# Performance work log

Measured on AMD Instinct MI355X. Metric: run time of the kernel, lower is better.

## Reference

```python
import jax, jax.numpy as jnp
import numpy as np

N, E, D = 50000, 800000, 128
H, C = 8, 16  # heads, hidden_per_head; H*C == D
NEG_SLOPE = 0.15


def setup_inputs() -> dict:
    key = jax.random.key(0)
    ks = jax.random.split(key, 8)
    x = jax.random.normal(ks[0], (N, D), dtype=jnp.float32)
    edge_index = jax.random.randint(ks[1], (2, E), 0, N, dtype=jnp.int32)
    s = 1.0 / np.sqrt(D)
    return {
        "x": x,
        "edge_index": edge_index,
        "ln_g": jnp.ones((D,), jnp.float32),
        "ln_b": jnp.zeros((D,), jnp.float32),
        "W_l": jax.random.normal(ks[2], (D, H * C), jnp.float32) * s,
        "b_l": jnp.zeros((H * C,), jnp.float32),
        "W_r": jax.random.normal(ks[3], (D, H * C), jnp.float32) * s,
        "b_r": jnp.zeros((H * C,), jnp.float32),
        "att": jax.random.normal(ks[4], (H, C), jnp.float32) * (1.0 / np.sqrt(C)),
        "bias": jnp.zeros((H * C,), jnp.float32),
    }


def _layernorm(x, g, b, eps=1e-5):
    mu = jnp.mean(x, axis=-1, keepdims=True)
    var = jnp.mean(jnp.square(x - mu), axis=-1, keepdims=True)
    return (x - mu) * jax.lax.rsqrt(var + eps) * g + b


def reference(x, edge_index, ln_g, ln_b, W_l, b_l, W_r, b_r, att, bias):
    src, dst = edge_index[0], edge_index[1]
    h = _layernorm(x, ln_g, ln_b)                      # [N, D]
    xl = (h @ W_l + b_l).reshape(N, H, C)              # source-side transform
    xr = (h @ W_r + b_r).reshape(N, H, C)              # target-side transform
    # GATv2 edge attention: leaky_relu(x_j + x_i) . att
    e = xl[src] + xr[dst]                              # [E, H, C]
    e_act = jnp.where(e > 0, e, NEG_SLOPE * e)
    alpha = jnp.einsum('ehc,hc->eh', e_act, att)       # [E, H]
    # segment softmax over edges grouped by destination node
    m = jax.ops.segment_max(alpha, dst, num_segments=N)   # [N, H]
    ex = jnp.exp(alpha - m[dst])                           # [E, H]
    denom = jax.ops.segment_sum(ex, dst, num_segments=N)  # [N, H]
    a = ex / (denom[dst] + 1e-16)                          # [E, H]
    # weighted message aggregation (scatter-add)
    msg = xl[src] * a[:, :, None]                          # [E, H, C]
    out = jax.ops.segment_sum(msg, dst, num_segments=N)   # [N, H, C]
    out = out.reshape(N, H * C) + bias
    h2 = jax.nn.relu(out)                                  # act='relu', dropout off (eval)
    return x + h2                                          # proj is Identity (in_dim == out_dim)
```

## Files before the change

### kernel.cpp

```cpp
#include <hip/hip_runtime.h>

typedef unsigned int uint32;
typedef __attribute__((ext_vector_type(4))) float f32x4;
typedef __attribute__((ext_vector_type(2))) float f32x2;
typedef __attribute__((ext_vector_type(8))) short bf16x8;

#define NEG_SLOPE 0.15f
#define GPB 2

__device__ __forceinline__ float2 bf2_to_f2(uint32 u) {
  union { uint32 i; float f; } a, b;
  a.i = u << 16;
  b.i = u & 0xffff0000u;
  return make_float2(a.f, b.f);
}

__device__ __forceinline__ f32x2 unpk(uint32 u) {
  union { uint32 i; float f; } lo, hi;
  lo.i = u << 16; hi.i = u & 0xffff0000u;
  f32x2 r; r.x = lo.f; r.y = hi.f; return r;
}

__device__ __forceinline__ float bf_to_f(unsigned short s) {
  union { uint32 i; float f; } u;
  u.i = ((uint32)s) << 16;
  return u.f;
}

__device__ __forceinline__ unsigned short f32_to_bf16(float f) {
  union { float f; uint32 i; } u; u.f = f;
  uint32 r = u.i + 0x7fffu + ((u.i >> 16) & 1u);
  return (unsigned short)(r >> 16);
}

__device__ __forceinline__ uint32 pack_bf2(float x, float y) {
  return (uint32)f32_to_bf16(x) | ((uint32)f32_to_bf16(y) << 16);
}

__device__ __forceinline__ float2 loadpair(const void* p, size_t i, int isbf) {
  if (isbf) return bf2_to_f2(((const uint32*)p)[i]);
  return ((const float2*)p)[i];
}

__device__ __forceinline__ float loadelem(const void* p, size_t i, int isbf) {
  if (isbf) return bf_to_f(((const unsigned short*)p)[i]);
  return ((const float*)p)[i];
}

__device__ __forceinline__ int get_isbf(const void* ln_g) {
  return ((const uint32*)ln_g)[0] != 0x3F800000u ? 1 : 0;
}

__device__ __forceinline__ float dpp_swap1(float x) {
  union { float f; int i; } u, r;
  u.f = x;
  r.i = __builtin_amdgcn_mov_dpp(u.i, 0xB1, 0xF, 0xF, false);
  return r.f;
}

__device__ __forceinline__ f32x2 pk_add(f32x2 a, f32x2 b) {
  f32x2 d;
  asm("v_pk_add_f32 %0, %1, %2" : "=v"(d) : "v"(a), "v"(b));
  return d;
}
__device__ __forceinline__ f32x2 pk_mul(f32x2 a, f32x2 b) {
  f32x2 d;
  asm("v_pk_mul_f32 %0, %1, %2" : "=v"(d) : "v"(a), "v"(b));
  return d;
}
__device__ __forceinline__ f32x2 pk_fma(f32x2 a, f32x2 b, f32x2 c) {
  f32x2 d;
  asm("v_pk_fma_f32 %0, %1, %2, %3" : "=v"(d) : "v"(a), "v"(b), "v"(c));
  return d;
}
__device__ __forceinline__ float exp2_raw(float x) {
  float r;
  asm("v_exp_f32 %0, %1" : "=v"(r) : "v"(x));
  return r;
}

__global__ __launch_bounds__(256) void prep_hist_k(
    const void* __restrict__ Wl, const void* __restrict__ Wr,
    const void* __restrict__ bl, const void* __restrict__ br,
    const void* __restrict__ att, const void* __restrict__ obias,
    const void* __restrict__ ln_g, const void* __restrict__ ln_b,
    unsigned short* __restrict__ Wt, float* __restrict__ c1,
    float* __restrict__ c2b, float* __restrict__ att_c,
    float* __restrict__ obias_c,
    const int* __restrict__ ei, int* __restrict__ cntg,
    int E, int Eb, int R)
{
  int b = blockIdx.x;
  if (b < 128) {
    int isbf = get_isbf(ln_g);
    int id = b * 256 + threadIdx.x;
    int n = id >> 7, k = id & 127;
    float g = loadelem(ln_g, k, isbf);
    float v = (n < 128) ? loadelem(Wl, (size_t)k * 128 + n, isbf)
                        : loadelem(Wr, (size_t)k * 128 + (n - 128), isbf);
    Wt[(size_t)n * 128 + k] = f32_to_bf16(g * v);
    if (id < 128) {
      att_c[id]   = loadelem(att, id, isbf) * 1.44269504088896f;
      obias_c[id] = loadelem(obias, id, isbf);
    }
  } else if (b < 192) {
    int isbf = get_isbf(ln_g);
    int w = threadIdx.x >> 6, lane = threadIdx.x & 63;
    int n = (b - 128) * 4 + w;
    const void* W = (n < 128) ? Wl : Wr;
    int nn = n & 127;
    float s1 = 0.f, s2 = 0.f;
    #pragma unroll
    for (int t = 0; t < 2; ++t) {
      int kk = t * 64 + lane;
      float wv = loadelem(W, (size_t)kk * 128 + nn, isbf);
      s1 += loadelem(ln_g, kk, isbf) * wv;
      s2 += loadelem(ln_b, kk, isbf) * wv;
    }
    #pragma unroll
    for (int off = 1; off < 64; off <<= 1) {
      s1 += __shfl_xor(s1, off, 64);
      s2 += __shfl_xor(s2, off, 64);
    }
    if (lane == 0) {
      c1[n] = s1;
      c2b[n] = s2 + ((n < 128) ? loadelem(bl, nn, isbf) : loadelem(br, nn, isbf));
    }
  } else {
    __shared__ int hist[256];
    int hb = b - 192, tid = threadIdx.x;
    hist[tid] = 0;
    __syncthreads();
    int startE = hb * Eb, endE = min(E, startE + Eb);
    const int* dp = ei + E;
    int nfull = (endE > startE) ? ((endE - startE) >> 2) : 0;
    for (int g = tid; g < nfull; g += 256) {
      int4 d = *(const int4*)(dp + startE + g * 4);
      atomicAdd(&hist[((uint32)d.x) >> 8], 1);
      atomicAdd(&hist[((uint32)d.y) >> 8], 1);
      atomicAdd(&hist[((uint32)d.z) >> 8], 1);
      atomicAdd(&hist[((uint32)d.w) >> 8], 1);
    }
    int rem0 = startE + nfull * 4;
    if (rem0 + tid < endE) atomicAdd(&hist[((uint32)dp[rem0 + tid]) >> 8], 1);
    __syncthreads();
    if (tid < R) cntg[tid * 256 + hb] = hist[tid];
  }
}

__global__ __launch_bounds__(1024) void scanA_k(const int* __restrict__ in,
    int* __restrict__ outl, int* __restrict__ psum, int n)
{
  __shared__ int wsum[16];
  int tid = threadIdx.x, lane = tid & 63, w = tid >> 6;
  int i = blockIdx.x * 1024 + tid;
  int v = (i < n) ? in[i] : 0;
  int xs = v;
  #pragma unroll
  for (int off = 1; off < 64; off <<= 1) {
    int y = __shfl_up(xs, off, 64);
    if (lane >= off) xs += y;
  }
  if (lane == 63) wsum[w] = xs;
  __syncthreads();
  if (w == 0) {
    int sv = (lane < 16) ? wsum[lane] : 0;
    int ss = sv;
    #pragma unroll
    for (int off = 1; off < 16; off <<= 1) {
      int y = __shfl_up(ss, off, 64);
      if (lane >= off) ss += y;
    }
    if (lane < 16) wsum[lane] = ss - sv;
    if (lane == 15) psum[blockIdx.x] = ss;
  }
  __syncthreads();
  if (i < n) outl[i] = wsum[w] + xs - v;
}

__device__ __forceinline__ void load_group(bf16x8* slot, const void* x,
                                           int isbf, int rl, int quad) {
  if (isbf) {
    const unsigned short* xp = (const unsigned short*)x + (size_t)rl * 128 + quad * 8;
    #pragma unroll
    for (int kc = 0; kc < 4; ++kc) slot[kc] = *(const bf16x8*)(xp + kc * 32);
  } else {
    const float* xp = (const float*)x + (size_t)rl * 128 + quad * 8;
    #pragma unroll
    for (int kc = 0; kc < 4; ++kc) {
      float4 a0 = *(const float4*)(xp + kc * 32);
      float4 a1 = *(const float4*)(xp + kc * 32 + 4);
      union { bf16x8 v; uint32 u[4]; } av;
      av.u[0] = pack_bf2(a0.x, a0.y);
      av.u[1] = pack_bf2(a0.z, a0.w);
      av.u[2] = pack_bf2(a1.x, a1.y);
      av.u[3] = pack_bf2(a1.z, a1.w);
      slot[kc] = av.v;
    }
  }
}

__global__ __launch_bounds__(256) void bin_gemm_k(
    const int* __restrict__ ei, const int* __restrict__ cbase,
    const int* __restrict__ psum, uint32* __restrict__ binned,
    int E, int Eb, int R, int nbScan,
    const void* __restrict__ x, const void* __restrict__ ln_g,
    const unsigned short* __restrict__ Wt,
    const float* __restrict__ c1, const float* __restrict__ c2b,
    unsigned short* __restrict__ xl, unsigned short* __restrict__ xr,
    int nrows)
{
  if (blockIdx.x < 256) {
    __shared__ int cur[256];
    __shared__ int spsum[64];
    int b = blockIdx.x, tid = threadIdx.x;
    if (tid < 64) {
      int v = (tid < nbScan) ? psum[tid] : 0;
      int xs = v;
      #pragma unroll
      for (int off = 1; off < 64; off <<= 1) {
        int y = __shfl_up(xs, off, 64);
        if (tid >= off) xs += y;
      }
      spsum[tid] = xs - v;
    }
    __syncthreads();
    if (tid < R) {
      int idx = tid * 256 + b;
      cur[tid] = cbase[idx] + spsum[idx >> 10];
    }
    __syncthreads();
    int startE = b * Eb, endE = min(E, startE + Eb);
    int nfull = (endE > startE) ? ((endE - startE) >> 2) : 0;
    for (int g = tid; g < nfull; g += 256) {
      int e = startE + g * 4;
      int4 s = *(const int4*)(ei + e);
      int4 d = *(const int4*)(ei + E + e);
      int p0 = atomicAdd(&cur[((uint32)d.x) >> 8], 1);
      binned[p0] = (uint32)s.x | (((uint32)d.x & 255u) << 16);
      int p1 = atomicAdd(&cur[((uint32)d.y) >> 8], 1);
      binned[p1] = (uint32)s.y | (((uint32)d.y & 255u) << 16);
      int p2 = atomicAdd(&cur[((uint32)d.z) >> 8], 1);
      binned[p2] = (uint32)s.z | (((uint32)d.z & 255u) << 16);
      int p3 = atomicAdd(&cur[((uint32)d.w) >> 8], 1);
      binned[p3] = (uint32)s.w | (((uint32)d.w & 255u) << 16);
    }
    int rem0 = startE + nfull * 4;
    if (rem0 + tid < endE) {
      int e = rem0 + tid;
      uint32 src = (uint32)ei[e], dst = (uint32)ei[E + e];
      int pos = atomicAdd(&cur[dst >> 8], 1);
      binned[pos] = src | ((dst & 255u) << 16);
    }
    return;
  }

  int bid  = blockIdx.x - 256;
  int isbf = get_isbf(ln_g);
  int lane = threadIdx.x & 63;
  int w    = threadIdx.x >> 6;
  int m16  = lane & 15;
  int quad = lane >> 4;
  int base = bid * (GPB * 16);

  bf16x8 araw[GPB][4];
  #pragma unroll
  for (int g2 = 0; g2 < GPB; ++g2) {
    int r = base + g2 * 16 + m16;
    if (r >= nrows) r = nrows - 1;
    load_group(araw[g2], x, isbf, r, quad);
  }

  bf16x8 bfrag[4][4];
  #pragma unroll
  for (int nt = 0; nt < 4; ++nt)
    #pragma unroll
    for (int kc = 0; kc < 4; ++kc)
      bfrag[nt][kc] = *(const bf16x8*)(
          Wt + (size_t)(w * 64 + nt * 16 + m16) * 128 + kc * 32 + quad * 8);

  float c1v[4], c2v[4];
  #pragma unroll
  for (int nt = 0; nt < 4; ++nt) {
    int col = w * 64 + nt * 16 + m16;
    c1v[nt] = c1[col];
    c2v[nt] = c2b[col];
  }

  unsigned short* dst = (w < 2) ? xl : xr;
  int cb = (w & 1) * 64;

  #pragma unroll
  for (int g2 = 0; g2 < GPB; ++g2) {
    bf16x8* A = araw[g2];

    float s = 0.f, s2 = 0.f;
    #pragma unroll
    for (int kc = 0; kc < 4; ++kc) {
      union { bf16x8 v; uint32 u[4]; } uu; uu.v = A[kc];
      #pragma unroll
      for (int j = 0; j < 4; ++j) {
        float2 t = bf2_to_f2(uu.u[j]);
        s += t.x + t.y;
        s2 += t.x * t.x + t.y * t.y;
      }
    }
    s  += __shfl_xor(s, 16, 64);  s2 += __shfl_xor(s2, 16, 64);
    s  += __shfl_xor(s, 32, 64);  s2 += __shfl_xor(s2, 32, 64);
    float mu  = s * (1.0f / 128.0f);
    float var = fmaxf(s2 * (1.0f / 128.0f) - mu * mu, 0.0f);
    float rs  = rsqrtf(var + 1e-5f);
    float rm  = rs * mu;

    f32x4 acc[4];
    #pragma unroll
    for (int nt = 0; nt < 4; ++nt) acc[nt] = (f32x4){0.f, 0.f, 0.f, 0.f};
    #pragma unroll
    for (int kc = 0; kc < 4; ++kc)
      #pragma unroll
      for (int nt = 0; nt < 4; ++nt)
        acc[nt] = __builtin_amdgcn_mfma_f32_16x16x32_bf16(A[kc], bfrag[nt][kc], acc[nt], 0, 0, 0);

    float rs_j[4], rm_j[4];
    #pragma unroll
    for (int j = 0; j < 4; ++j) {
      rs_j[j] = __shfl(rs, quad * 4 + j, 64);
      rm_j[j] = __shfl(rm, quad * 4 + j, 64);
    }

    #pragma unroll
    for (int nt = 0; nt < 4; ++nt) {
      #pragma unroll
      for (int j = 0; j < 4; ++j) {
        int r = base + g2 * 16 + quad * 4 + j;
        if (r < nrows)
          dst[(size_t)r * 128 + cb + nt * 16 + m16] =
              f32_to_bf16(rs_j[j] * acc[nt][j] - rm_j[j] * c1v[nt] + c2v[nt]);
      }
    }
  }
}

__global__ __launch_bounds__(1024) void rangesort_k(
    const uint32* __restrict__ binned, const int* __restrict__ cbase,
    const int* __restrict__ psum,
    int* __restrict__ starts, unsigned short* __restrict__ csr16,
    int E, int N, int R, int nbScan)
{
  __shared__ int hist[256];
  __shared__ int wsum[4];
  __shared__ int cur[256];
  __shared__ int spsum[64];
  int r = blockIdx.x;
  int tid = threadIdx.x, lane = tid & 63, w = tid >> 6;

  if (tid < 64) {
    int pv = (tid < nbScan) ? psum[tid] : 0;
    int pxs = pv;
    #pragma unroll
    for (int off = 1; off < 64; off <<= 1) {
      int y = __shfl_up(pxs, off, 64);
      if (tid >= off) pxs += y;
    }
    spsum[tid] = pxs - pv;
  }
  if (tid < 256) hist[tid] = 0;
  __syncthreads();

  int i0 = r * 256;
  int segStart = cbase[i0] + spsum[i0 >> 10];
  int segEnd;
  if (r + 1 < R) {
    int i1 = (r + 1) * 256;
    segEnd = cbase[i1] + spsum[i1 >> 10];
  } else {
    segEnd = E;
  }
  if (r == 0) {
    if (tid == 0) starts[N] = E;
    if (tid < 32) csr16[E + tid] = 0;
  }

  for (int i = segStart + tid; i < segEnd; i += 1024)
    atomicAdd(&hist[(binned[i] >> 16) & 255u], 1);
  __syncthreads();

  int v = 0, xs = 0;
  if (tid < 256) {
    v = hist[tid];
    xs = v;
    #pragma unroll
    for (int off = 1; off < 64; off <<= 1) {
      int y = __shfl_up(xs, off, 64);
      if (lane >= off) xs += y;
    }
    if (lane == 63) wsum[w] = xs;
  }
  __syncthreads();
  if (tid < 256) {
    int woff = 0;
    #pragma unroll
    for (int i = 0; i < 4; ++i) if (i < w) woff += wsum[i];
    int st = segStart + woff + xs - v;
    int node = (r << 8) + tid;
    if (node < N) starts[node] = st;
    cur[tid] = st;
  }
  __syncthreads();

  for (int i = segStart + tid; i < segEnd; i += 1024) {
    uint32 pk = binned[i];
    int d = (pk >> 16) & 255u;
    int pos = atomicAdd(&cur[d], 1);
    csr16[pos] = (unsigned short)(pk & 0xffffu);
  }
}

__global__ __launch_bounds__(256) void agg_k(
    const uint32* __restrict__ xl32,
    const uint32* __restrict__ xr32,
    const int* __restrict__ starts, const unsigned short* __restrict__ csr16,
    const void* __restrict__ x, const void* __restrict__ ln_g,
    const float* __restrict__ att_c, const float* __restrict__ obias_c,
    void* __restrict__ out, int n)
{
  int node = blockIdx.x * 4 + (threadIdx.x >> 6);
  if (node >= n) return;
  int isbf = get_isbf(ln_g);
  int lane = threadIdx.x & 63;
  int q    = lane >> 4;
  int sub  = lane & 15;

  uint4 xru = *(const uint4*)(xr32 + (size_t)node * 64 + sub * 4);
  f32x2 xr0 = unpk(xru.x), xr1 = unpk(xru.y), xr2 = unpk(xru.z), xr3 = unpk(xru.w);
  const f32x2* atp = (const f32x2*)(att_c + sub * 8);
  f32x2 t0 = atp[0], t1 = atp[1], t2 = atp[2], t3 = atp[3];
  f32x2 ns; ns.x = NEG_SLOPE; ns.y = NEG_SLOPE;

  float lsum = 0.f;
  f32x2 ac[4];
  #pragma unroll
  for (int i = 0; i < 4; ++i) { ac[i].x = 0.f; ac[i].y = 0.f; }

  int p0 = __builtin_amdgcn_readfirstlane(starts[node]);
  int p1 = __builtin_amdgcn_readfirstlane(starts[node + 1]);

#define AGG_BODY(XU, OK) do { \
    f32x2 a0 = unpk((XU).x), a1 = unpk((XU).y), a2 = unpk((XU).z), a3 = unpk((XU).w); \
    f32x2 e0 = pk_add(a0, xr0), e1 = pk_add(a1, xr1); \
    f32x2 e2 = pk_add(a2, xr2), e3 = pk_add(a3, xr3); \
    f32x2 m0 = pk_mul(e0, ns), m1 = pk_mul(e1, ns); \
    f32x2 m2 = pk_mul(e2, ns), m3 = pk_mul(e3, ns); \
    e0.x = fmaxf(e0.x, m0.x); e0.y = fmaxf(e0.y, m0.y); \
    e1.x = fmaxf(e1.x, m1.x); e1.y = fmaxf(e1.y, m1.y); \
    e2.x = fmaxf(e2.x, m2.x); e2.y = fmaxf(e2.y, m2.y); \
    e3.x = fmaxf(e3.x, m3.x); e3.y = fmaxf(e3.y, m3.y); \
    f32x2 dt = pk_mul(e0, t0); \
    dt = pk_fma(e1, t1, dt); \
    dt = pk_fma(e2, t2, dt); \
    dt = pk_fma(e3, t3, dt); \
    float dot = dt.x + dt.y; \
    dot += dpp_swap1(dot); \
    float pw = (OK) ? exp2_raw(dot) : 0.f; \
    lsum += pw; \
    f32x2 pw2; pw2.x = pw; pw2.y = pw; \
    ac[0] = pk_fma(pw2, a0, ac[0]); \
    ac[1] = pk_fma(pw2, a1, ac[1]); \
    ac[2] = pk_fma(pw2, a2, ac[2]); \
    ac[3] = pk_fma(pw2, a3, ac[3]); \
  } while (0)

  if (p0 < p1) {
    uint32 so = (uint32)(sub * 4);
    const unsigned short* csp = csr16 + p0 + q;
    uint32 j0 = csp[0];
    uint32 j1 = csp[4];
    uint32 j2 = csp[8];
    uint32 j3 = csp[12];
    uint4 xu0 = *(const uint4*)(xl32 + (size_t)(j0 * 64u + so));
    uint4 xu1 = *(const uint4*)(xl32 + (size_t)(j1 * 64u + so));
    int pq   = p0 + q;
    int p1m4 = p1 - 4;
    for (int p = p0; p < p1; p += 8) {
      uint4 xA = xu0;
      xu0 = *(const uint4*)(xl32 + (size_t)(j2 * 64u + so));
      j2  = csp[16];
      AGG_BODY(xA, pq < p1);
      uint4 xB = xu1;
      xu1 = *(const uint4*)(xl32 + (size_t)(j3 * 64u + so));
      j3  = csp[20];
      AGG_BODY(xB, pq < p1m4);
      csp += 8;
      pq  += 8;
    }
  }
#undef AGG_BODY

  lsum += __shfl_xor(lsum, 16, 64);
  lsum += __shfl_xor(lsum, 32, 64);
  #pragma unroll
  for (int i = 0; i < 4; ++i) {
    ac[i].x += __shfl_xor(ac[i].x, 16, 64);
    ac[i].x += __shfl_xor(ac[i].x, 32, 64);
    ac[i].y += __shfl_xor(ac[i].y, 16, 64);
    ac[i].y += __shfl_xor(ac[i].y, 32, 64);
  }

  if (q == 0) {
    float inv = 1.0f / (lsum + 1e-16f);
    float4 b0 = *(const float4*)(obias_c + sub * 8);
    float4 b1 = *(const float4*)(obias_c + sub * 8 + 4);
    float2 rx[4];
    #pragma unroll
    for (int i = 0; i < 4; ++i)
      rx[i] = loadpair(x, (size_t)node * 64 + sub * 4 + i, isbf);
    float o0 = rx[0].x + fmaxf(ac[0].x * inv + b0.x, 0.f);
    float o1 = rx[0].y + fmaxf(ac[0].y * inv + b0.y, 0.f);
    float o2 = rx[1].x + fmaxf(ac[1].x * inv + b0.z, 0.f);
    float o3 = rx[1].y + fmaxf(ac[1].y * inv + b0.w, 0.f);
    float o4 = rx[2].x + fmaxf(ac[2].x * inv + b1.x, 0.f);
    float o5 = rx[2].y + fmaxf(ac[2].y * inv + b1.y, 0.f);
    float o6 = rx[3].x + fmaxf(ac[3].x * inv + b1.z, 0.f);
    float o7 = rx[3].y + fmaxf(ac[3].y * inv + b1.w, 0.f);
    if (isbf) {
      uint4 ov;
      ov.x = pack_bf2(o0, o1); ov.y = pack_bf2(o2, o3);
      ov.z = pack_bf2(o4, o5); ov.w = pack_bf2(o6, o7);
      *(uint4*)((uint32*)out + (size_t)node * 64 + sub * 4) = ov;
    } else {
      float4 f0 = make_float4(o0, o1, o2, o3);
      float4 f1 = make_float4(o4, o5, o6, o7);
      *(float4*)((float*)out + (size_t)node * 128 + sub * 8) = f0;
      *(float4*)((float*)out + (size_t)node * 128 + sub * 8 + 4) = f1;
    }
  }
}

static inline char* align16(char* p) {
  return (char*)(((uintptr_t)p + 15) & ~(uintptr_t)15);
}

extern "C" void kernel_launch(void* const* d_in, const int* in_sizes, int n_in,
                              void* d_out, int out_size, void* d_ws, size_t ws_size,
                              hipStream_t stream) {
  const void* x    = d_in[0];
  const int*  ei   = (const int*)d_in[1];
  const void* ln_g = d_in[2];
  const void* ln_b = d_in[3];
  const void* Wl   = d_in[4];
  const void* bl   = d_in[5];
  const void* Wr   = d_in[6];
  const void* br   = d_in[7];
  const void* att  = d_in[8];
  const void* bias = d_in[9];

  int N = in_sizes[0] / 128;
  int E = in_sizes[1] / 2;
  int R = (N + 255) >> 8;
  int L = R * 256;
  int Eb = (((E + 255) / 256) + 3) & ~3;

  char* ws = (char*)d_ws;
  unsigned short* xl = (unsigned short*)ws; ws = align16(ws + (size_t)N * 128 * 2);
  unsigned short* xr = (unsigned short*)ws; ws = align16(ws + (size_t)N * 128 * 2);
  unsigned short* Wt = (unsigned short*)ws; ws = align16(ws + 256 * 128 * 2);
  float* c1      = (float*)ws;              ws = align16(ws + 256 * 4);
  float* c2b     = (float*)ws;              ws = align16(ws + 256 * 4);
  float* att_c   = (float*)ws;              ws = align16(ws + 128 * 4);
  float* obias_c = (float*)ws;              ws = align16(ws + 128 * 4);
  int* cntg      = (int*)ws;                ws = align16(ws + (size_t)L * 4);
  int* cbase     = (int*)ws;                ws = align16(ws + (size_t)L * 4);
  int* psum      = (int*)ws;                ws = align16(ws + 64 * 4);
  int* starts    = (int*)ws;                ws = align16(ws + (size_t)(N + 1) * 4);
  uint32* binned = (uint32*)ws;             ws = align16(ws + (size_t)E * 4);
  unsigned short* csr16 = (unsigned short*)ws; ws = align16(ws + (size_t)(E + 32) * 2);

  int nbScan = (L + 1023) / 1024;
  int nGemmB = (N + GPB * 16 - 1) / (GPB * 16);

  hipLaunchKernelGGL(prep_hist_k, dim3(448), dim3(256), 0, stream,
                     Wl, Wr, bl, br, att, bias, ln_g, ln_b,
                     Wt, c1, c2b, att_c, obias_c,
                     ei, cntg, E, Eb, R);
  hipLaunchKernelGGL(scanA_k, dim3(nbScan), dim3(1024), 0, stream, cntg, cbase, psum, L);
  hipLaunchKernelGGL(bin_gemm_k, dim3(256 + nGemmB), dim3(256), 0, stream,
                     ei, cbase, psum, binned, E, Eb, R, nbScan,
                     x, ln_g, Wt, c1, c2b, xl, xr, N);
  hipLaunchKernelGGL(rangesort_k, dim3(R), dim3(1024), 0, stream,
                     binned, cbase, psum, starts, csr16, E, N, R, nbScan);
  hipLaunchKernelGGL(agg_k, dim3((N + 3) / 4), dim3(256), 0, stream,
                     (const uint32*)xl, (const uint32*)xr, starts, csr16,
                     x, ln_g, att_c, obias_c, d_out, N);
}
```

Measured before the change: 173.9 us.

## Remap aggregation lanes to 8 edges x 8 lanes per wave, 32B per lane

The aggregation kernel now processes 8 edges per iteration with 8 lanes per edge, each lane holding a full 16-channel head (two 16-byte loads). This removes the cross-lane DPP reduction for the attention dot product and changes the software prefetch to a single-stage double buffer with clamped indices. Blocks shrink to 128 threads (2 nodes each). Per-lane register pressure doubles and the final reduction needs an extra shuffle stage; fewer edges are in flight per lane.

```diff
diff --git a/kernel.cpp b/kernel.cpp
--- a/kernel.cpp
+++ b/kernel.cpp
@@ -49,13 +49,6 @@
 
 __device__ __forceinline__ int get_isbf(const void* ln_g) {
   return ((const uint32*)ln_g)[0] != 0x3F800000u ? 1 : 0;
-}
-
-__device__ __forceinline__ float dpp_swap1(float x) {
-  union { float f; int i; } u, r;
-  u.f = x;
-  r.i = __builtin_amdgcn_mov_dpp(u.i, 0xB1, 0xF, 0xF, false);
-  return r.f;
 }
 
 __device__ __forceinline__ f32x2 pk_add(f32x2 a, f32x2 b) {
@@ -378,7 +371,7 @@
   }
   if (r == 0) {
     if (tid == 0) starts[N] = E;
-    if (tid < 32) csr16[E + tid] = 0;
+    if (tid < 64) csr16[E + tid] = 0;
   }
 
   for (int i = segStart + tid; i < segEnd; i += 1024)
@@ -416,7 +409,7 @@
   }
 }
 
-__global__ __launch_bounds__(256) void agg_k(
+__global__ __launch_bounds__(128) void agg_k(
     const uint32* __restrict__ xl32,
     const uint32* __restrict__ xr32,
     const int* __restrict__ starts, const unsigned short* __restrict__ csr16,
@@ -424,43 +417,56 @@
     const float* __restrict__ att_c, const float* __restrict__ obias_c,
     void* __restrict__ out, int n)
 {
-  int node = blockIdx.x * 4 + (threadIdx.x >> 6);
+  int node = blockIdx.x * 2 + (threadIdx.x >> 6);
   if (node >= n) return;
   int isbf = get_isbf(ln_g);
   int lane = threadIdx.x & 63;
-  int q    = lane >> 4;
-  int sub  = lane & 15;
-
-  uint4 xru = *(const uint4*)(xr32 + (size_t)node * 64 + sub * 4);
-  f32x2 xr0 = unpk(xru.x), xr1 = unpk(xru.y), xr2 = unpk(xru.z), xr3 = unpk(xru.w);
-  const f32x2* atp = (const f32x2*)(att_c + sub * 8);
+  int q    = lane >> 3;
+  int s8   = lane & 7;
+
+  const uint32* xrp = xr32 + (size_t)node * 64 + s8 * 8;
+  uint4 xru0 = *(const uint4*)xrp;
+  uint4 xru1 = *(const uint4*)(xrp + 4);
+  f32x2 xr0 = unpk(xru0.x), xr1 = unpk(xru0.y), xr2 = unpk(xru0.z), xr3 = unpk(xru0.w);
+  f32x2 xr4 = unpk(xru1.x), xr5 = unpk(xru1.y), xr6 = unpk(xru1.z), xr7 = unpk(xru1.w);
+  const f32x2* atp = (const f32x2*)(att_c + s8 * 16);
   f32x2 t0 = atp[0], t1 = atp[1], t2 = atp[2], t3 = atp[3];
+  f32x2 t4 = atp[4], t5 = atp[5], t6 = atp[6], t7 = atp[7];
   f32x2 ns; ns.x = NEG_SLOPE; ns.y = NEG_SLOPE;
 
   float lsum = 0.f;
-  f32x2 ac[4];
+  f32x2 ac[8];
   #pragma unroll
-  for (int i = 0; i < 4; ++i) { ac[i].x = 0.f; ac[i].y = 0.f; }
+  for (int i = 0; i < 8; ++i) { ac[i].x = 0.f; ac[i].y = 0.f; }
 
   int p0 = __builtin_amdgcn_readfirstlane(starts[node]);
   int p1 = __builtin_amdgcn_readfirstlane(starts[node + 1]);
 
-#define AGG_BODY(XU, OK) do { \
+#define AGG_BODY(XU, XV, OK) do { \
     f32x2 a0 = unpk((XU).x), a1 = unpk((XU).y), a2 = unpk((XU).z), a3 = unpk((XU).w); \
+    f32x2 a4 = unpk((XV).x), a5 = unpk((XV).y), a6 = unpk((XV).z), a7 = unpk((XV).w); \
     f32x2 e0 = pk_add(a0, xr0), e1 = pk_add(a1, xr1); \
     f32x2 e2 = pk_add(a2, xr2), e3 = pk_add(a3, xr3); \
+    f32x2 e4 = pk_add(a4, xr4), e5 = pk_add(a5, xr5); \
+    f32x2 e6 = pk_add(a6, xr6), e7 = pk_add(a7, xr7); \
     f32x2 m0 = pk_mul(e0, ns), m1 = pk_mul(e1, ns); \
     f32x2 m2 = pk_mul(e2, ns), m3 = pk_mul(e3, ns); \
+    f32x2 m4 = pk_mul(e4, ns), m5 = pk_mul(e5, ns); \
+    f32x2 m6 = pk_mul(e6, ns), m7 = pk_mul(e7, ns); \
     e0.x = fmaxf(e0.x, m0.x); e0.y = fmaxf(e0.y, m0.y); \
     e1.x = fmaxf(e1.x, m1.x); e1.y = fmaxf(e1.y, m1.y); \
     e2.x = fmaxf(e2.x, m2.x); e2.y = fmaxf(e2.y, m2.y); \
     e3.x = fmaxf(e3.x, m3.x); e3.y = fmaxf(e3.y, m3.y); \
-    f32x2 dt = pk_mul(e0, t0); \
-    dt = pk_fma(e1, t1, dt); \
-    dt = pk_fma(e2, t2, dt); \
-    dt = pk_fma(e3, t3, dt); \
-    float dot = dt.x + dt.y; \
-    dot += dpp_swap1(dot); \
+    e4.x = fmaxf(e4.x, m4.x); e4.y = fmaxf(e4.y, m4.y); \
+    e5.x = fmaxf(e5.x, m5.x); e5.y = fmaxf(e5.y, m5.y); \
+    e6.x = fmaxf(e6.x, m6.x); e6.y = fmaxf(e6.y, m6.y); \
+    e7.x = fmaxf(e7.x, m7.x); e7.y = fmaxf(e7.y, m7.y); \
+    f32x2 dA = pk_mul(e0, t0); dA = pk_fma(e1, t1, dA); \
+    f32x2 dB = pk_mul(e2, t2); dB = pk_fma(e3, t3, dB); \
+    f32x2 dC = pk_mul(e4, t4); dC = pk_fma(e5, t5, dC); \
+    f32x2 dD = pk_mul(e6, t6); dD = pk_fma(e7, t7, dD); \
+    dA = pk_add(dA, dB); dC = pk_add(dC, dD); dA = pk_add(dA, dC); \
+    float dot = dA.x + dA.y; \
     float pw = (OK) ? exp2_raw(dot) : 0.f; \
     lsum += pw; \
     f32x2 pw2; pw2.x = pw; pw2.y = pw; \
@@ -468,70 +474,79 @@
     ac[1] = pk_fma(pw2, a1, ac[1]); \
     ac[2] = pk_fma(pw2, a2, ac[2]); \
     ac[3] = pk_fma(pw2, a3, ac[3]); \
+    ac[4] = pk_fma(pw2, a4, ac[4]); \
+    ac[5] = pk_fma(pw2, a5, ac[5]); \
+    ac[6] = pk_fma(pw2, a6, ac[6]); \
+    ac[7] = pk_fma(pw2, a7, ac[7]); \
   } while (0)
 
   if (p0 < p1) {
-    uint32 so = (uint32)(sub * 4);
+    uint32 so = (uint32)(s8 * 8);
     const unsigned short* csp = csr16 + p0 + q;
+    int pq = p0 + q;
     uint32 j0 = csp[0];
-    uint32 j1 = csp[4];
-    uint32 j2 = csp[8];
-    uint32 j3 = csp[12];
-    uint4 xu0 = *(const uint4*)(xl32 + (size_t)(j0 * 64u + so));
-    uint4 xu1 = *(const uint4*)(xl32 + (size_t)(j1 * 64u + so));
-    int pq   = p0 + q;
-    int p1m4 = p1 - 4;
-    for (int p = p0; p < p1; p += 8) {
-      uint4 xA = xu0;
-      xu0 = *(const uint4*)(xl32 + (size_t)(j2 * 64u + so));
-      j2  = csp[16];
-      AGG_BODY(xA, pq < p1);
-      uint4 xB = xu1;
-      xu1 = *(const uint4*)(xl32 + (size_t)(j3 * 64u + so));
-      j3  = csp[20];
-      AGG_BODY(xB, pq < p1m4);
+    if (pq >= p1) j0 = 0u;
+    uint32 j1 = csp[8];
+    const uint32* rp = xl32 + ((size_t)j0 * 64u + so);
+    uint4 xu = *(const uint4*)rp;
+    uint4 xv = *(const uint4*)(rp + 4);
+    for (int p = p0; ; p += 8) {
+      int more = (p + 8 < p1);
+      uint32 j2 = csp[16];
+      uint4 nxu, nxv;
+      if (more) {
+        uint32 jv = (pq + 8 < p1) ? j1 : 0u;
+        const uint32* rq = xl32 + ((size_t)jv * 64u + so);
+        nxu = *(const uint4*)rq;
+        nxv = *(const uint4*)(rq + 4);
+      }
+      AGG_BODY(xu, xv, pq < p1);
+      if (!more) break;
+      xu = nxu; xv = nxv;
+      j1 = j2;
       csp += 8;
       pq  += 8;
     }
   }
 #undef AGG_BODY
 
+  lsum += __shfl_xor(lsum, 8, 64);
   lsum += __shfl_xor(lsum, 16, 64);
   lsum += __shfl_xor(lsum, 32, 64);
   #pragma unroll
-  for (int i = 0; i < 4; ++i) {
+  for (int i = 0; i < 8; ++i) {
+    ac[i].x += __shfl_xor(ac[i].x, 8, 64);
     ac[i].x += __shfl_xor(ac[i].x, 16, 64);
     ac[i].x += __shfl_xor(ac[i].x, 32, 64);
+    ac[i].y += __shfl_xor(ac[i].y, 8, 64);
     ac[i].y += __shfl_xor(ac[i].y, 16, 64);
     ac[i].y += __shfl_xor(ac[i].y, 32, 64);
   }
 
   if (q == 0) {
     float inv = 1.0f / (lsum + 1e-16f);
-    float4 b0 = *(const float4*)(obias_c + sub * 8);
-    float4 b1 = *(const float4*)(obias_c + sub * 8 + 4);
-    float2 rx[4];
-    #pragma unroll
-    for (int i = 0; i < 4; ++i)
-      rx[i] = loadpair(x, (size_t)node * 64 + sub * 4 + i, isbf);
-    float o0 = rx[0].x + fmaxf(ac[0].x * inv + b0.x, 0.f);
-    float o1 = rx[0].y + fmaxf(ac[0].y * inv + b0.y, 0.f);
-    float o2 = rx[1].x + fmaxf(ac[1].x * inv + b0.z, 0.f);
-    float o3 = rx[1].y + fmaxf(ac[1].y * inv + b0.w, 0.f);
-    float o4 = rx[2].x + fmaxf(ac[2].x * inv + b1.x, 0.f);
-    float o5 = rx[2].y + fmaxf(ac[2].y * inv + b1.y, 0.f);
-    float o6 = rx[3].x + fmaxf(ac[3].x * inv + b1.z, 0.f);
-    float o7 = rx[3].y + fmaxf(ac[3].y * inv + b1.w, 0.f);
+    const float* obp = obias_c + s8 * 16;
+    float oo[16];
+    #pragma unroll
+    for (int i = 0; i < 8; ++i) {
+      float2 rxi = loadpair(x, (size_t)node * 64 + s8 * 8 + i, isbf);
+      oo[2 * i]     = rxi.x + fmaxf(ac[i].x * inv + obp[2 * i],     0.f);
+      oo[2 * i + 1] = rxi.y + fmaxf(ac[i].y * inv + obp[2 * i + 1], 0.f);
+    }
     if (isbf) {
-      uint4 ov;
-      ov.x = pack_bf2(o0, o1); ov.y = pack_bf2(o2, o3);
-      ov.z = pack_bf2(o4, o5); ov.w = pack_bf2(o6, o7);
-      *(uint4*)((uint32*)out + (size_t)node * 64 + sub * 4) = ov;
+      uint4 ov0, ov1;
+      ov0.x = pack_bf2(oo[0],  oo[1]);  ov0.y = pack_bf2(oo[2],  oo[3]);
+      ov0.z = pack_bf2(oo[4],  oo[5]);  ov0.w = pack_bf2(oo[6],  oo[7]);
+      ov1.x = pack_bf2(oo[8],  oo[9]);  ov1.y = pack_bf2(oo[10], oo[11]);
+      ov1.z = pack_bf2(oo[12], oo[13]); ov1.w = pack_bf2(oo[14], oo[15]);
+      uint4* op = (uint4*)((uint32*)out + (size_t)node * 64 + s8 * 8);
+      op[0] = ov0; op[1] = ov1;
     } else {
-      float4 f0 = make_float4(o0, o1, o2, o3);
-      float4 f1 = make_float4(o4, o5, o6, o7);
-      *(float4*)((float*)out + (size_t)node * 128 + sub * 8) = f0;
-      *(float4*)((float*)out + (size_t)node * 128 + sub * 8 + 4) = f1;
+      float4* op = (float4*)((float*)out + (size_t)node * 128 + s8 * 16);
+      op[0] = make_float4(oo[0],  oo[1],  oo[2],  oo[3]);
+      op[1] = make_float4(oo[4],  oo[5],  oo[6],  oo[7]);
+      op[2] = make_float4(oo[8],  oo[9],  oo[10], oo[11]);
+      op[3] = make_float4(oo[12], oo[13], oo[14], oo[15]);
     }
   }
 }
@@ -573,7 +588,7 @@
   int* psum      = (int*)ws;                ws = align16(ws + 64 * 4);
   int* starts    = (int*)ws;                ws = align16(ws + (size_t)(N + 1) * 4);
   uint32* binned = (uint32*)ws;             ws = align16(ws + (size_t)E * 4);
-  unsigned short* csr16 = (unsigned short*)ws; ws = align16(ws + (size_t)(E + 32) * 2);
+  unsigned short* csr16 = (unsigned short*)ws; ws = align16(ws + (size_t)(E + 64) * 2);
 
   int nbScan = (L + 1023) / 1024;
   int nGemmB = (N + GPB * 16 - 1) / (GPB * 16);
@@ -588,7 +603,7 @@
                      x, ln_g, Wt, c1, c2b, xl, xr, N);
   hipLaunchKernelGGL(rangesort_k, dim3(R), dim3(1024), 0, stream,
                      binned, cbase, psum, starts, csr16, E, N, R, nbScan);
-  hipLaunchKernelGGL(agg_k, dim3((N + 3) / 4), dim3(256), 0, stream,
+  hipLaunchKernelGGL(agg_k, dim3((N + 1) / 2), dim3(128), 0, stream,
                      (const uint32*)xl, (const uint32*)xr, starts, csr16,
                      x, ln_g, att_c, obias_c, d_out, N);
 }
```

Result: slower. 195.1 us (+12.2%).

## Replace two-level binned CSR build with direct global-atomic counting sort

Applied to the files above, without the earlier changes.

Replaces the bucketed histogram, block scan, binning and range-sort pipeline with per-node global atomic counts, a single-block scan over all nodes, and a direct atomic scatter of sources into the CSR array, fused with the GEMM launch. This drops one kernel launch and the intermediate binned buffer pass. In exchange it relies on global atomics with contention on random destinations, a serial single-block scan of 50k counts, and an extra memset. The edge order within each node becomes nondeterministic, as before.

```diff
diff --git a/kernel.cpp b/kernel.cpp
--- a/kernel.cpp
+++ b/kernel.cpp
@@ -79,7 +79,7 @@
   return r;
 }
 
-__global__ __launch_bounds__(256) void prep_hist_k(
+__global__ __launch_bounds__(256) void prep_cnt_k(
     const void* __restrict__ Wl, const void* __restrict__ Wr,
     const void* __restrict__ bl, const void* __restrict__ br,
     const void* __restrict__ att, const void* __restrict__ obias,
@@ -87,8 +87,8 @@
     unsigned short* __restrict__ Wt, float* __restrict__ c1,
     float* __restrict__ c2b, float* __restrict__ att_c,
     float* __restrict__ obias_c,
-    const int* __restrict__ ei, int* __restrict__ cntg,
-    int E, int Eb, int R)
+    const int* __restrict__ ei, int* __restrict__ cnt,
+    int E, int Eb)
 {
   int b = blockIdx.x;
   if (b < 128) {
@@ -127,35 +127,36 @@
       c2b[n] = s2 + ((n < 128) ? loadelem(bl, nn, isbf) : loadelem(br, nn, isbf));
     }
   } else {
-    __shared__ int hist[256];
     int hb = b - 192, tid = threadIdx.x;
-    hist[tid] = 0;
-    __syncthreads();
     int startE = hb * Eb, endE = min(E, startE + Eb);
     const int* dp = ei + E;
     int nfull = (endE > startE) ? ((endE - startE) >> 2) : 0;
     for (int g = tid; g < nfull; g += 256) {
       int4 d = *(const int4*)(dp + startE + g * 4);
-      atomicAdd(&hist[((uint32)d.x) >> 8], 1);
-      atomicAdd(&hist[((uint32)d.y) >> 8], 1);
-      atomicAdd(&hist[((uint32)d.z) >> 8], 1);
-      atomicAdd(&hist[((uint32)d.w) >> 8], 1);
+      atomicAdd(&cnt[d.x], 1);
+      atomicAdd(&cnt[d.y], 1);
+      atomicAdd(&cnt[d.z], 1);
+      atomicAdd(&cnt[d.w], 1);
     }
     int rem0 = startE + nfull * 4;
-    if (rem0 + tid < endE) atomicAdd(&hist[((uint32)dp[rem0 + tid]) >> 8], 1);
-    __syncthreads();
-    if (tid < R) cntg[tid * 256 + hb] = hist[tid];
-  }
-}
-
-__global__ __launch_bounds__(1024) void scanA_k(const int* __restrict__ in,
-    int* __restrict__ outl, int* __restrict__ psum, int n)
+    if (rem0 + tid < endE) atomicAdd(&cnt[dp[rem0 + tid]], 1);
+  }
+}
+
+__global__ __launch_bounds__(1024) void scan1_k(
+    const int* __restrict__ cnt, int* __restrict__ starts, int* __restrict__ cur,
+    unsigned short* __restrict__ csr16, int N, int E)
 {
   __shared__ int wsum[16];
   int tid = threadIdx.x, lane = tid & 63, w = tid >> 6;
-  int i = blockIdx.x * 1024 + tid;
-  int v = (i < n) ? in[i] : 0;
-  int xs = v;
+  int C = (N + 1023) >> 10;
+  int base = tid * C;
+  int s = 0;
+  for (int i = 0; i < C; ++i) {
+    int idx = base + i;
+    if (idx < N) s += cnt[idx];
+  }
+  int xs = s;
   #pragma unroll
   for (int off = 1; off < 64; off <<= 1) {
     int y = __shfl_up(xs, off, 64);
@@ -172,10 +173,20 @@
       if (lane >= off) ss += y;
     }
     if (lane < 16) wsum[lane] = ss - sv;
-    if (lane == 15) psum[blockIdx.x] = ss;
   }
   __syncthreads();
-  if (i < n) outl[i] = wsum[w] + xs - v;
+  int run = wsum[w] + xs - s;
+  for (int i = 0; i < C; ++i) {
+    int idx = base + i;
+    if (idx < N) {
+      int c = cnt[idx];
+      starts[idx] = run;
+      cur[idx] = run;
+      run += c;
+    }
+  }
+  if (tid == 1023) starts[N] = E;
+  if (tid < 64) csr16[E + tid] = 0;
 }
 
 __device__ __forceinline__ void load_group(bf16x8* slot, const void* x,
@@ -200,62 +211,41 @@
   }
 }
 
-__global__ __launch_bounds__(256) void bin_gemm_k(
-    const int* __restrict__ ei, const int* __restrict__ cbase,
-    const int* __restrict__ psum, uint32* __restrict__ binned,
-    int E, int Eb, int R, int nbScan,
+__global__ __launch_bounds__(256) void scat_gemm_k(
+    const int* __restrict__ ei, int* __restrict__ cur,
+    unsigned short* __restrict__ csr16, int E,
     const void* __restrict__ x, const void* __restrict__ ln_g,
     const unsigned short* __restrict__ Wt,
     const float* __restrict__ c1, const float* __restrict__ c2b,
     unsigned short* __restrict__ xl, unsigned short* __restrict__ xr,
     int nrows)
 {
-  if (blockIdx.x < 256) {
-    __shared__ int cur[256];
-    __shared__ int spsum[64];
-    int b = blockIdx.x, tid = threadIdx.x;
-    if (tid < 64) {
-      int v = (tid < nbScan) ? psum[tid] : 0;
-      int xs = v;
-      #pragma unroll
-      for (int off = 1; off < 64; off <<= 1) {
-        int y = __shfl_up(xs, off, 64);
-        if (tid >= off) xs += y;
-      }
-      spsum[tid] = xs - v;
-    }
-    __syncthreads();
-    if (tid < R) {
-      int idx = tid * 256 + b;
-      cur[tid] = cbase[idx] + spsum[idx >> 10];
-    }
-    __syncthreads();
-    int startE = b * Eb, endE = min(E, startE + Eb);
-    int nfull = (endE > startE) ? ((endE - startE) >> 2) : 0;
-    for (int g = tid; g < nfull; g += 256) {
-      int e = startE + g * 4;
+  if (blockIdx.x < 64) {
+    int tid = blockIdx.x * 256 + threadIdx.x;
+    int nfull = E >> 2;
+    for (int g = tid; g < nfull; g += 16384) {
+      int e = g * 4;
       int4 s = *(const int4*)(ei + e);
       int4 d = *(const int4*)(ei + E + e);
-      int p0 = atomicAdd(&cur[((uint32)d.x) >> 8], 1);
-      binned[p0] = (uint32)s.x | (((uint32)d.x & 255u) << 16);
-      int p1 = atomicAdd(&cur[((uint32)d.y) >> 8], 1);
-      binned[p1] = (uint32)s.y | (((uint32)d.y & 255u) << 16);
-      int p2 = atomicAdd(&cur[((uint32)d.z) >> 8], 1);
-      binned[p2] = (uint32)s.z | (((uint32)d.z & 255u) << 16);
-      int p3 = atomicAdd(&cur[((uint32)d.w) >> 8], 1);
-      binned[p3] = (uint32)s.w | (((uint32)d.w & 255u) << 16);
-    }
-    int rem0 = startE + nfull * 4;
-    if (rem0 + tid < endE) {
+      int p0 = atomicAdd(&cur[d.x], 1);
+      csr16[p0] = (unsigned short)s.x;
+      int p1 = atomicAdd(&cur[d.y], 1);
+      csr16[p1] = (unsigned short)s.y;
+      int p2 = atomicAdd(&cur[d.z], 1);
+      csr16[p2] = (unsigned short)s.z;
+      int p3 = atomicAdd(&cur[d.w], 1);
+      csr16[p3] = (unsigned short)s.w;
+    }
+    int rem0 = nfull * 4;
+    if (rem0 + tid < E) {
       int e = rem0 + tid;
-      uint32 src = (uint32)ei[e], dst = (uint32)ei[E + e];
-      int pos = atomicAdd(&cur[dst >> 8], 1);
-      binned[pos] = src | ((dst & 255u) << 16);
+      int pos = atomicAdd(&cur[ei[E + e]], 1);
+      csr16[pos] = (unsigned short)ei[e];
     }
     return;
   }
 
-  int bid  = blockIdx.x - 256;
+  int bid  = blockIdx.x - 64;
   int isbf = get_isbf(ln_g);
   int lane = threadIdx.x & 63;
   int w    = threadIdx.x >> 6;
@@ -338,81 +328,6 @@
               f32_to_bf16(rs_j[j] * acc[nt][j] - rm_j[j] * c1v[nt] + c2v[nt]);
       }
     }
-  }
-}
-
-__global__ __launch_bounds__(1024) void rangesort_k(
-    const uint32* __restrict__ binned, const int* __restrict__ cbase,
-    const int* __restrict__ psum,
-    int* __restrict__ starts, unsigned short* __restrict__ csr16,
-    int E, int N, int R, int nbScan)
-{
-  __shared__ int hist[256];
-  __shared__ int wsum[4];
-  __shared__ int cur[256];
-  __shared__ int spsum[64];
-  int r = blockIdx.x;
-  int tid = threadIdx.x, lane = tid & 63, w = tid >> 6;
-
-  if (tid < 64) {
-    int pv = (tid < nbScan) ? psum[tid] : 0;
-    int pxs = pv;
-    #pragma unroll
-    for (int off = 1; off < 64; off <<= 1) {
-      int y = __shfl_up(pxs, off, 64);
-      if (tid >= off) pxs += y;
-    }
-    spsum[tid] = pxs - pv;
-  }
-  if (tid < 256) hist[tid] = 0;
-  __syncthreads();
-
-  int i0 = r * 256;
-  int segStart = cbase[i0] + spsum[i0 >> 10];
-  int segEnd;
-  if (r + 1 < R) {
-    int i1 = (r + 1) * 256;
-    segEnd = cbase[i1] + spsum[i1 >> 10];
-  } else {
-    segEnd = E;
-  }
-  if (r == 0) {
-    if (tid == 0) starts[N] = E;
-    if (tid < 32) csr16[E + tid] = 0;
-  }
-
-  for (int i = segStart + tid; i < segEnd; i += 1024)
-    atomicAdd(&hist[(binned[i] >> 16) & 255u], 1);
-  __syncthreads();
-
-  int v = 0, xs = 0;
-  if (tid < 256) {
-    v = hist[tid];
-    xs = v;
-    #pragma unroll
-    for (int off = 1; off < 64; off <<= 1) {
-      int y = __shfl_up(xs, off, 64);
-      if (lane >= off) xs += y;
-    }
-    if (lane == 63) wsum[w] = xs;
-  }
-  __syncthreads();
-  if (tid < 256) {
-    int woff = 0;
-    #pragma unroll
-    for (int i = 0; i < 4; ++i) if (i < w) woff += wsum[i];
-    int st = segStart + woff + xs - v;
-    int node = (r << 8) + tid;
-    if (node < N) starts[node] = st;
-    cur[tid] = st;
-  }
-  __syncthreads();
-
-  for (int i = segStart + tid; i < segEnd; i += 1024) {
-    uint32 pk = binned[i];
-    int d = (pk >> 16) & 255u;
-    int pos = atomicAdd(&cur[d], 1);
-    csr16[pos] = (unsigned short)(pk & 0xffffu);
   }
 }
 
@@ -556,8 +471,6 @@
 
   int N = in_sizes[0] / 128;
   int E = in_sizes[1] / 2;
-  int R = (N + 255) >> 8;
-  int L = R * 256;
   int Eb = (((E + 255) / 256) + 3) & ~3;
 
   char* ws = (char*)d_ws;
@@ -568,26 +481,23 @@
   float* c2b     = (float*)ws;              ws = align16(ws + 256 * 4);
   float* att_c   = (float*)ws;              ws = align16(ws + 128 * 4);
   float* obias_c = (float*)ws;              ws = align16(ws + 128 * 4);
-  int* cntg      = (int*)ws;                ws = align16(ws + (size_t)L * 4);
-  int* cbase     = (int*)ws;                ws = align16(ws + (size_t)L * 4);
-  int* psum      = (int*)ws;                ws = align16(ws + 64 * 4);
+  int* cnt       = (int*)ws;                ws = align16(ws + (size_t)N * 4);
   int* starts    = (int*)ws;                ws = align16(ws + (size_t)(N + 1) * 4);
-  uint32* binned = (uint32*)ws;             ws = align16(ws + (size_t)E * 4);
-  unsigned short* csr16 = (unsigned short*)ws; ws = align16(ws + (size_t)(E + 32) * 2);
-
-  int nbScan = (L + 1023) / 1024;
+  int* cur       = (int*)ws;                ws = align16(ws + (size_t)N * 4);
+  unsigned short* csr16 = (unsigned short*)ws; ws = align16(ws + (size_t)(E + 64) * 2);
+
   int nGemmB = (N + GPB * 16 - 1) / (GPB * 16);
 
-  hipLaunchKernelGGL(prep_hist_k, dim3(448), dim3(256), 0, stream,
+  hipMemsetAsync(cnt, 0, (size_t)N * 4, stream);
+  hipLaunchKernelGGL(prep_cnt_k, dim3(448), dim3(256), 0, stream,
                      Wl, Wr, bl, br, att, bias, ln_g, ln_b,
                      Wt, c1, c2b, att_c, obias_c,
-                     ei, cntg, E, Eb, R);
-  hipLaunchKernelGGL(scanA_k, dim3(nbScan), dim3(1024), 0, stream, cntg, cbase, psum, L);
-  hipLaunchKernelGGL(bin_gemm_k, dim3(256 + nGemmB), dim3(256), 0, stream,
-                     ei, cbase, psum, binned, E, Eb, R, nbScan,
+                     ei, cnt, E, Eb);
+  hipLaunchKernelGGL(scan1_k, dim3(1), dim3(1024), 0, stream,
+                     cnt, starts, cur, csr16, N, E);
+  hipLaunchKernelGGL(scat_gemm_k, dim3(64 + nGemmB), dim3(256), 0, stream,
+                     ei, cur, csr16, E,
                      x, ln_g, Wt, c1, c2b, xl, xr, N);
-  hipLaunchKernelGGL(rangesort_k, dim3(R), dim3(1024), 0, stream,
-                     binned, cbase, psum, starts, csr16, E, N, R, nbScan);
   hipLaunchKernelGGL(agg_k, dim3((N + 3) / 4), dim3(256), 0, stream,
                      (const uint32*)xl, (const uint32*)xr, starts, csr16,
                      x, ln_g, att_c, obias_c, d_out, N);
```

Measured after the change: 347.8 us. 100.0% more time.
